# Optimization experiments

Hardware: AMD Instinct MI355X
Metric: run time of the kernel (lower is better)

Reference implementation:

```python
import jax, jax.numpy as jnp
import numpy as np

_R, _C = 64, 64
_N = _R * _C
_SEC_PER_A = 31556926.0
_K = 0.01        # sheet_conductivity
_ALPHA = 1.25    # sheet_flow_exp
_HR = 0.1        # bedrock_step_height
_LR = 2.0        # cavity_spacing
_A = 5e-25       # cavity_closure_coeff
_NEXP = 3        # Glen exponent


def _build_grid():
    idx = np.arange(_N).reshape(_R, _C)
    tail = np.concatenate([idx[:, :-1].ravel(), idx[:-1, :].ravel()]).astype(np.int32)
    head = np.concatenate([idx[:, 1:].ravel(), idx[1:, :].ravel()]).astype(np.int32)
    L = tail.size
    links_at_node = -np.ones((_N, 4), np.int32)
    adj = -np.ones((_N, 4), np.int32)
    cnt = np.zeros(_N, np.int32)
    for l in range(L):
        for a, b in ((tail[l], head[l]), (head[l], tail[l])):
            links_at_node[a, cnt[a]] = l
            adj[a, cnt[a]] = b
            cnt[a] += 1
    r, c = np.divmod(np.arange(_N), _C)
    status = ((r == 0) | (r == _R - 1) | (c == 0) | (c == _C - 1)).astype(np.int32)
    return tail, head, links_at_node, adj, status


def setup_inputs():
    key = jax.random.key(0)
    k = jax.random.split(key, 8)
    tail, head, links_at_node, adj, status = _build_grid()
    L = tail.size
    bedrock = jax.random.uniform(k[0], (_N,), jnp.float32, 0.0, 500.0)
    ice_thk = jax.random.uniform(k[1], (_N,), jnp.float32, 100.0, 1000.0)
    overburden = 917.0 * 9.81 * ice_thk
    base_potential = 1000.0 * 9.81 * bedrock + overburden
    potential = base_potential - 0.3 * overburden + 1e3 * jax.random.normal(k[2], (_N,), jnp.float32)
    sheet_thickness = jax.random.uniform(k[3], (_N,), jnp.float32, 0.01, 0.1)
    sliding_velocity = jax.random.uniform(k[4], (L,), jnp.float32, 10.0, 100.0)
    specific_melt_rate = jax.random.uniform(k[5], (_N,), jnp.float32, 1e-7, 1e-6)
    link_length = jnp.full((L,), 100.0, jnp.float32)
    adj_j = jnp.asarray(adj)
    # mean over ALL 4 slots, padded entries contribute 0 (matches original jnp.mean)
    adj_pot = jnp.mean(jnp.where(adj_j != -1, base_potential[adj_j], 0.0), axis=1)
    inflow = jnp.where(base_potential > adj_pot, 1, -1) * (jnp.asarray(status) > 0)
    return dict(
        base_potential=base_potential,
        overburden_pressure=overburden,
        specific_melt_rate=specific_melt_rate,
        sheet_thickness=sheet_thickness,
        potential=potential,
        sliding_velocity=sliding_velocity,
        link_length=link_length,
        link_tail=jnp.asarray(tail),
        link_head=jnp.asarray(head),
        links_at_node=jnp.asarray(links_at_node),
        inflow_outflow=inflow.astype(jnp.int32),
        dt=3600,
    )


def reference(base_potential, overburden_pressure, specific_melt_rate, sheet_thickness,
              potential, sliding_velocity, link_length, link_tail, link_head,
              links_at_node, inflow_outflow, dt):
    N = base_potential.shape[0]
    t, h = link_tail, link_head
    # --- elliptic operator assembly (per-link, scatter into dense [N,N]) ---
    sheets = 0.5 * (sheet_thickness[t] + sheet_thickness[h])
    inv_grad = jnp.abs((potential[t] - potential[h]) / link_length) ** (-0.5)
    c = -_K * sheets ** _ALPHA * link_length * inv_grad  # symmetric link coefficient (<0)
    dir_row = inflow_outflow == 1  # Dirichlet rows
    ct = jnp.where(dir_row[t], 0.0, c)  # contribution into row tail
    ch = jnp.where(dir_row[h], 0.0, c)  # contribution into row head
    M = (jnp.zeros((N, N), base_potential.dtype)
         .at[t, h].add(ct).at[h, t].add(ch)
         .at[t, t].add(-ct).at[h, h].add(-ch))
    M = jnp.where(dir_row[:, None], jnp.eye(N, dtype=M.dtype), M)
    forcing = jnp.where(dir_row, base_potential - overburden_pressure, specific_melt_rate)
    new_potential = jnp.linalg.solve(M, forcing)
    # --- sheet thickness: map_mean_of_links_to_node then Newton on node-local ODE ---
    valid = links_at_node != -1
    lv = (sliding_velocity / _SEC_PER_A)[links_at_node]  # [N,4]
    sliding = jnp.abs(jnp.sum(jnp.where(valid, lv, 0.0), axis=1)
                      / jnp.maximum(valid.sum(axis=1), 1))
    pressure = base_potential - new_potential
    dtf = jnp.asarray(dt, base_potential.dtype)
    # residual r(h) = h - h0 - dt*(sliding*(HR-h)/LR - A*P^n*h) is LINEAR in h,
    # so Newton converges in one exact step -> closed form:
    new_h = (sheet_thickness + dtf * sliding * _HR / _LR) / (
        1.0 + dtf * (sliding / _LR + _A * pressure ** _NEXP))
    return new_potential, new_h
```

## Files before the change

### kernel.cpp

```cpp
#include <hip/hip_runtime.h>
#include <math.h>


#define NT    512
#define NPT   8
#define NN    4096
#define NC    1024
#define NCC   256
#define CCIT  20
#define MAXIT 40

__global__ __launch_bounds__(NT, 1)
void sds_solver(const float* __restrict__ base_pot,
                const float* __restrict__ ovb,
                const float* __restrict__ melt,
                const float* __restrict__ sheet,
                const float* __restrict__ pot,
                const float* __restrict__ svel,
                const float* __restrict__ llen,
                const int*   __restrict__ ltail,
                const int*   __restrict__ lhead,
                const int*   __restrict__ lan,
                const int*   __restrict__ inflow,
                const int*   __restrict__ dt_raw,
                float* __restrict__ out,
                int N, int L)
{
    __shared__ __align__(16) float ZL0[2112], ZH0[2112];
    __shared__ __align__(16) float ZL1[2112], ZH1[2112];
    __shared__ __align__(16) float cW[NN], cE[NN], cN[NN], cS[NN];
    __shared__ __align__(16) float CB[32 + NC + 32];
    __shared__ __align__(16) float CB2[32 + NC + 32];
    __shared__ __align__(16) float EB[32 + NC + 32];
    __shared__ __align__(16) float ccb[NCC];
    __shared__ __align__(16) float cWc_s[NC], cEc_s[NC], cNc_s[NC], cSc_s[NC], dc_s[NC];
    __shared__ double redp[32], redg[16];

    const int tid  = threadIdx.x;
    const int lane = tid & 63;
    const int wid  = tid >> 6;
    const int m    = tid * NPT;

    if (N != NN || L != 8064) return;

    const int dti = dt_raw[0];
    const float as_f = __int_as_float(dti);
    const double dtf = (as_f > 0.5f && as_f < 1.0e12f) ? (double)as_f : (double)dti;

    const float invthf = 0.8f;
    const float c1f = 0.2195122f, c2f = 0.9756098f;
    const float wA = 1.75f;

    {
        const float4 z4 = make_float4(0.f, 0.f, 0.f, 0.f);
        #pragma unroll
        for (int i = tid; i < NN/4; i += NT) {
            ((float4*)cW)[i] = z4; ((float4*)cE)[i] = z4;
            ((float4*)cN)[i] = z4; ((float4*)cS)[i] = z4;
        }
        if (tid < 32) {
            ZL0[tid]=0.f; ZL0[2080+tid]=0.f; ZH0[tid]=0.f; ZH0[2080+tid]=0.f;
            ZL1[tid]=0.f; ZL1[2080+tid]=0.f; ZH1[tid]=0.f; ZH1[2080+tid]=0.f;
            CB[tid]=0.f;  CB[32+NC+tid]=0.f;
            CB2[tid]=0.f; CB2[32+NC+tid]=0.f;
            EB[tid]=0.f;  EB[32+NC+tid]=0.f;
        }
    }
    __syncthreads();

    for (int l = tid; l < 8064; l += NT) {
        int t, h;
        if (l < 4032) {
            const int r = l / 63;
            const int c2 = l - r * 63;
            t = (r << 6) + c2; h = t + 1;
        } else {
            t = l - 4032; h = t + 64;
        }
        const float sheets = 0.5f * (sheet[t] + sheet[h]);
        const float len = llen[l];
        const float grad = fabsf((pot[t] - pot[h]) / len);
        const float c = -0.01f * (sheets * sqrtf(sqrtf(sheets))) * len / sqrtf(grad);
        const bool dt_ = (inflow[t] == 1);
        const bool dh_ = (inflow[h] == 1);
        if (l < 4032) { cE[t] = dt_ ? 0.f : c; cW[h] = dh_ ? 0.f : c; }
        else          { cS[t] = dt_ ? 0.f : c; cN[h] = dh_ ? 0.f : c; }
    }
    __syncthreads();

    float cw[NPT], ce[NPT], cn[NPT], cs[NPT], dgf[NPT], invdf[NPT];
    double bb[NPT], gg[NPT], xv[NPT], rv[NPT];
    bool dirf[NPT];
    auto ldco = [&]() {
        const float4 w0 = *(const float4*)&cW[m], w1 = *(const float4*)&cW[m+4];
        const float4 e0 = *(const float4*)&cE[m], e1 = *(const float4*)&cE[m+4];
        const float4 n0 = *(const float4*)&cN[m], n1 = *(const float4*)&cN[m+4];
        const float4 s0 = *(const float4*)&cS[m], s1 = *(const float4*)&cS[m+4];
        cw[0]=w0.x;cw[1]=w0.y;cw[2]=w0.z;cw[3]=w0.w;cw[4]=w1.x;cw[5]=w1.y;cw[6]=w1.z;cw[7]=w1.w;
        ce[0]=e0.x;ce[1]=e0.y;ce[2]=e0.z;ce[3]=e0.w;ce[4]=e1.x;ce[5]=e1.y;ce[6]=e1.z;ce[7]=e1.w;
        cn[0]=n0.x;cn[1]=n0.y;cn[2]=n0.z;cn[3]=n0.w;cn[4]=n1.x;cn[5]=n1.y;cn[6]=n1.z;cn[7]=n1.w;
        cs[0]=s0.x;cs[1]=s0.y;cs[2]=s0.z;cs[3]=s0.w;cs[4]=s1.x;cs[5]=s1.y;cs[6]=s1.z;cs[7]=s1.w;
    };
    ldco();
    double gsum = 0.0, gcnt = 0.0;
    #pragma unroll
    for (int k = 0; k < NPT; ++k) {
        const int n = m + k;
        const bool dir = (inflow[n] == 1);
        const double g = (double)base_pot[n] - (double)ovb[n];
        const double d = -((double)cw[k] + (double)ce[k] + (double)cn[k] + (double)cs[k]);
        const double dg = (dir || d == 0.0) ? 1.0 : d;
        dgf[k] = (float)dg; invdf[k] = (float)(1.0 / dg);
        bb[k] = dir ? g : (double)melt[n];
        gg[k] = g; dirf[k] = dir;
        if (dir) { gsum += g; gcnt += 1.0; }
    }
    {
        #pragma unroll
        for (int off = 32; off > 0; off >>= 1) {
            gsum += __shfl_down(gsum, off, 64);
            gcnt += __shfl_down(gcnt, off, 64);
        }
        if (lane == 0) { redg[2*wid] = gsum; redg[2*wid+1] = gcnt; }
        __syncthreads();
        gsum = 0.0; gcnt = 0.0;
        #pragma unroll
        for (int w = 0; w < NT/64; ++w) { gsum += redg[2*w]; gcnt += redg[2*w+1]; }
    }
    const double gmean = gsum / (gcnt > 0.0 ? gcnt : 1.0);

    auto stz = [&](float* L_, float* H_, const float* v) {
        *(float4*)&L_[32 + 4*tid] = make_float4(v[0], v[1], v[2], v[3]);
        *(float4*)&H_[32 + 4*tid] = make_float4(v[4], v[5], v[6], v[7]);
    };
    float qf[NPT];
    auto spmv = [&](const float* L_, const float* H_, const float* vr) {
        const float4 uL = *(const float4*)&L_[4*tid];
        const float4 uH = *(const float4*)&H_[4*tid];
        const float4 dL = *(const float4*)&L_[64 + 4*tid];
        const float4 dH = *(const float4*)&H_[64 + 4*tid];
        const float lw = __shfl_up(vr[7], 1, 64);
        const float re = __shfl_down(vr[0], 1, 64);
        const float up[NPT] = {uL.x,uL.y,uL.z,uL.w,uH.x,uH.y,uH.z,uH.w};
        const float dn[NPT] = {dL.x,dL.y,dL.z,dL.w,dH.x,dH.y,dH.z,dH.w};
        #pragma unroll
        for (int k = 0; k < NPT; ++k) {
            const float wv = k ? vr[k-1] : lw;
            const float ev = (k < NPT-1) ? vr[k+1] : re;
            qf[k] = dgf[k]*vr[k] + cw[k]*wv + ce[k]*ev + cn[k]*up[k] + cs[k]*dn[k];
        }
    };
    auto fread0 = [&](int n) -> float {
        const int off = 32 + ((n >> 3) << 2) + (n & 3);
        return (n & 4) ? ZH0[off] : ZL0[off];
    };

    {
        float x0r[NPT];
        #pragma unroll
        for (int k = 0; k < NPT; ++k) {
            const float x0f = (float)(dirf[k] ? gg[k] : gmean);
            xv[k] = (double)x0f; x0r[k] = x0f;
        }
        stz(ZL0, ZH0, x0r); __syncthreads();
        spmv(ZL0, ZH0, x0r);
        #pragma unroll
        for (int k = 0; k < NPT; ++k)
            rv[k] = dirf[k] ? 0.0 : (bb[k] - (double)qf[k]);
    }
    __syncthreads();

    {
        #pragma unroll
        for (int k = 0; k < NPT; ++k) {
            const int n = m + k;
            if ((n & 63) != 0  && inflow[n-1]  == 1) cW[n] = 0.f;
            if ((n & 63) != 63 && inflow[n+1]  == 1) cE[n] = 0.f;
            if (n >= 64        && inflow[n-64] == 1) cN[n] = 0.f;
            if (n < NN-64      && inflow[n+64] == 1) cS[n] = 0.f;
        }
        float dgfF[NPT];
        #pragma unroll
        for (int k = 0; k < NPT; ++k) dgfF[k] = dirf[k] ? 0.f : dgf[k];
        stz(ZL0, ZH0, dgfF);
    }
    __syncthreads();
    ldco();

    #pragma unroll
    for (int q = 0; q < 2; ++q) {
        const int I = 2*tid + q;
        const int R = tid >> 4, C = I & 31;
        const int na = 128*R + 2*C, nb = na+1, nc_ = na+64, nd = na+65;
        cEc_s[I] = cE[nb] + cE[nd];
        cWc_s[I] = cW[na] + cW[nc_];
        cNc_s[I] = cN[na] + cN[nb];
        cSc_s[I] = cS[nc_] + cS[nd];
        const float d = fread0(na)+fread0(nb)+fread0(nc_)+fread0(nd)
                      + 2.0f*(cE[na] + cE[nc_] + cS[na] + cS[nb]);
        dc_s[I] = (d > 0.f) ? d : 1.0f;
    }
    __syncthreads();

    float cwc[2], cec[2], cnc[2], csc[2], dcr[2], invdc[2];
    {
        float2 t;
        t = *(float2*)&cWc_s[2*tid]; cwc[0]=t.x; cwc[1]=t.y;
        t = *(float2*)&cEc_s[2*tid]; cec[0]=t.x; cec[1]=t.y;
        t = *(float2*)&cNc_s[2*tid]; cnc[0]=t.x; cnc[1]=t.y;
        t = *(float2*)&cSc_s[2*tid]; csc[0]=t.x; csc[1]=t.y;
        t = *(float2*)&dc_s[2*tid];  dcr[0]=t.x; dcr[1]=t.y;
        invdc[0] = 1.0f/dcr[0]; invdc[1] = 1.0f/dcr[1];
    }
    float cwcc[4], cecc[4], cncc[4], cscc[4], dccr[4], invdcc[4];
    if (tid < 64) {
        #pragma unroll
        for (int j = 0; j < 4; ++j) {
            const int J = 4*tid + j;
            const int Rc = J >> 4, Cc = J & 15;
            const int IA = 64*Rc + 2*Cc, IB = IA+1, IC = IA+32, ID = IA+33;
            cecc[j] = cEc_s[IB] + cEc_s[ID];
            cwcc[j] = cWc_s[IA] + cWc_s[IC];
            cncc[j] = cNc_s[IA] + cNc_s[IB];
            cscc[j] = cSc_s[IC] + cSc_s[ID];
            const float d = dc_s[IA]+dc_s[IB]+dc_s[IC]+dc_s[ID]
                          + 2.0f*(cEc_s[IA] + cEc_s[IC] + cSc_s[IA] + cSc_s[IB]);
            dccr[j] = (d > 0.f) ? d : 1.0f;
            invdcc[j] = 1.0f/dccr[j];
        }
    }
    float c1cc[CCIT+1], c2cc[CCIT+1], invthcc;
    {
        const double a = 8e-3, b2 = 2.0;
        const double th = 0.5*(b2+a), de = 0.5*(b2-a), s1 = th/de;
        double rp = 1.0/s1;
        for (int j = 1; j <= CCIT; ++j) {
            const double rj = 1.0/(2.0*s1 - rp);
            c1cc[j] = (float)(rj*rp);
            c2cc[j] = (float)(2.0*rj/de);
            rp = rj;
        }
        invthcc = (float)(1.0/th);
    }
    auto cspmv = [&](const float* B_, float v0, float v1, float& q0, float& q1) {
        const float2 up = *(const float2*)&B_[2*tid];
        const float2 dn = *(const float2*)&B_[64 + 2*tid];
        const float wv = __shfl_up(v1, 1, 64);
        const float ev = __shfl_down(v0, 1, 64);
        q0 = dcr[0]*v0 + cwc[0]*wv + cec[0]*v1 + cnc[0]*up.x + csc[0]*dn.x;
        q1 = dcr[1]*v1 + cwc[1]*v0 + cec[1]*ev + cnc[1]*up.y + csc[1]*dn.y;
    };

    double rho_prev = 0.0, pap = 0.0, tol = 0.0;
    double pv[NPT], sv[NPT], rpv[NPT];
    #pragma unroll
    for (int k = 0; k < NPT; ++k) { pv[k]=0.0; sv[k]=0.0; rpv[k]=0.0; }

    for (int it = 0; it < MAXIT; ++it) {
        float f0[NPT], d0[NPT], d1[NPT], zpre[NPT];
        #pragma unroll
        for (int k = 0; k < NPT; ++k) { f0[k] = (float)rv[k] * invdf[k]; d0[k] = f0[k] * invthf; }
        stz(ZL0, ZH0, d0); __syncthreads();
        spmv(ZL0, ZH0, d0);
        #pragma unroll
        for (int k = 0; k < NPT; ++k) {
            const float f1 = f0[k] - qf[k]*invdf[k];
            d1[k] = c1f*d0[k] + c2f*f1;
            zpre[k] = d0[k] + d1[k];
            f0[k] = f1;
        }
        stz(ZL1, ZH1, d1); __syncthreads();
        spmv(ZL1, ZH1, d1);

        float r1[NPT], r1p[NPT];
        #pragma unroll
        for (int k = 0; k < NPT; ++k) {
            const float fres = f0[k] - qf[k]*invdf[k];
            r1[k] = dirf[k] ? 0.f : dgf[k]*fres;
        }
        #pragma unroll
        for (int k = 0; k < NPT; ++k) r1p[k] = __shfl_down(r1[k], 8, 64);
        if ((tid & 8) == 0) {
            float4 rc4;
            rc4.x = r1[0]+r1[1]+r1p[0]+r1p[1];
            rc4.y = r1[2]+r1[3]+r1p[2]+r1p[3];
            rc4.z = r1[4]+r1[5]+r1p[4]+r1p[5];
            rc4.w = r1[6]+r1[7]+r1p[6]+r1p[7];
            const int I0 = 32*(tid >> 4) + 4*(tid & 7);
            *(float4*)&CB2[32 + I0] = rc4;
        }
        __syncthreads();

        float rc[2], f0c[2], d0c[2], d1c[2], qc0, qc1;
        {
            const float2 rcl = *(const float2*)&CB2[32 + 2*tid];
            rc[0] = rcl.x; rc[1] = rcl.y;
        }
        #pragma unroll
        for (int q = 0; q < 2; ++q) {
            f0c[q] = rc[q] * invdc[q];
            d0c[q] = f0c[q] * invthf;
        }
        *(float2*)&CB[32 + 2*tid] = make_float2(d0c[0], d0c[1]);
        __syncthreads();
        cspmv(CB, d0c[0], d0c[1], qc0, qc1);
        {
            const float f1a = f0c[0] - qc0*invdc[0];
            const float f1b = f0c[1] - qc1*invdc[1];
            d1c[0] = c1f*d0c[0] + c2f*f1a;
            d1c[1] = c1f*d0c[1] + c2f*f1b;
            f0c[0] = f1a; f0c[1] = f1b;
        }
        *(float2*)&CB2[32 + 2*tid] = make_float2(d1c[0], d1c[1]);
        __syncthreads();
        cspmv(CB2, d1c[0], d1c[1], qc0, qc1);
        {
            const float fra = f0c[0] - qc0*invdc[0];
            const float frb = f0c[1] - qc1*invdc[1];
            *(float2*)&CB[32 + 2*tid] = make_float2(dcr[0]*fra, dcr[1]*frb);
        }
        __syncthreads();

        if (tid < 64) {
            float fr[4], dr[4], zc[4];
            #pragma unroll
            for (int j = 0; j < 4; ++j) {
                const int J = 4*tid + j;
                const int IA = 64*(J >> 4) + 2*(J & 15);
                const float rcc = CB[32+IA] + CB[32+IA+1] + CB[32+IA+32] + CB[32+IA+33];
                fr[j] = rcc * invdcc[j];
                dr[j] = fr[j] * invthcc;
                zc[j] = dr[j];
            }
            for (int s = 1; s <= CCIT; ++s) {
                float nv[4], sv2[4], qcc[4];
                #pragma unroll
                for (int j = 0; j < 4; ++j) {
                    nv[j]  = __shfl_up(dr[j], 4, 64);
                    sv2[j] = __shfl_down(dr[j], 4, 64);
                }
                const float wv = __shfl_up(dr[3], 1, 64);
                const float ev = __shfl_down(dr[0], 1, 64);
                #pragma unroll
                for (int j = 0; j < 4; ++j) {
                    const float wj = j ? dr[j-1] : wv;
                    const float ej = (j < 3) ? dr[j+1] : ev;
                    qcc[j] = dccr[j]*dr[j] + cwcc[j]*wj + cecc[j]*ej
                           + cncc[j]*nv[j] + cscc[j]*sv2[j];
                }
                #pragma unroll
                for (int j = 0; j < 4; ++j) {
                    fr[j] -= qcc[j] * invdcc[j];
                    dr[j]  = c1cc[s]*dr[j] + c2cc[s]*fr[j];
                    zc[j] += dr[j];
                }
            }
            *(float4*)&ccb[4*tid] = make_float4(zc[0], zc[1], zc[2], zc[3]);
        }
        __syncthreads();

        const float ecv = wA * ccb[16*(tid >> 5) + (tid & 15)];
        float zmc[2] = { d0c[0] + d1c[0] + ecv, d0c[1] + d1c[1] + ecv };
        *(float2*)&CB2[32 + 2*tid] = make_float2(zmc[0], zmc[1]);
        __syncthreads();
        cspmv(CB2, zmc[0], zmc[1], qc0, qc1);
        float fmc[2] = { (rc[0]-qc0)*invdc[0], (rc[1]-qc1)*invdc[1] };
        float d0p[2] = { fmc[0]*invthf, fmc[1]*invthf };
        *(float2*)&CB[32 + 2*tid] = make_float2(d0p[0], d0p[1]);
        __syncthreads();
        cspmv(CB, d0p[0], d0p[1], qc0, qc1);
        {
            const float f1a = fmc[0] - qc0*invdc[0];
            const float f1b = fmc[1] - qc1*invdc[1];
            const float efa = zmc[0] + c1f*d0p[0] + c2f*f1a + d0p[0];
            const float efb = zmc[1] + c1f*d0p[1] + c2f*f1b + d0p[1];
            *(float2*)&EB[32 + 2*tid] = make_float2(efa, efb);
        }
        __syncthreads();

        const float4 e4 = *(const float4*)&EB[32 + 32*(tid >> 4) + (tid & 7)*4];
        const float* e4p = (const float*)&e4;
        float zmid[NPT], zf[NPT];
        #pragma unroll
        for (int k = 0; k < NPT; ++k)
            zmid[k] = zpre[k] + (dirf[k] ? 0.f : wA * e4p[k >> 1]);
        stz(ZL1, ZH1, zmid); __syncthreads();
        spmv(ZL1, ZH1, zmid);
        float fmid[NPT], d0q[NPT];
        #pragma unroll
        for (int k = 0; k < NPT; ++k) {
            fmid[k] = (float)rv[k]*invdf[k] - qf[k]*invdf[k];
            d0q[k]  = fmid[k] * invthf;
        }
        stz(ZL0, ZH0, d0q); __syncthreads();
        spmv(ZL0, ZH0, d0q);
        #pragma unroll
        for (int k = 0; k < NPT; ++k) {
            const float f1 = fmid[k] - qf[k]*invdf[k];
            zf[k] = zmid[k] + d0q[k] + c1f*d0q[k] + c2f*f1;
        }
        stz(ZL1, ZH1, zf); __syncthreads();
        spmv(ZL1, ZH1, zf);

        double rho_n = 0.0, rzp = 0.0, zw = 0.0, pw = 0.0;
        #pragma unroll
        for (int k = 0; k < NPT; ++k) {
            const double zk = (double)zf[k], wk = (double)qf[k];
            rho_n += rv[k]  * zk;
            rzp   += rpv[k] * zk;
            zw    += zk * wk;
            pw    += pv[k] * wk;
        }
        #pragma unroll
        for (int off = 32; off > 0; off >>= 1) {
            rho_n += __shfl_down(rho_n, off, 64);
            rzp   += __shfl_down(rzp,   off, 64);
            zw    += __shfl_down(zw,    off, 64);
            pw    += __shfl_down(pw,    off, 64);
        }
        if (lane == 0) {
            redp[4*wid] = rho_n; redp[4*wid+1] = rzp;
            redp[4*wid+2] = zw;  redp[4*wid+3] = pw;
        }
        __syncthreads();
        rho_n = 0.0; rzp = 0.0; zw = 0.0; pw = 0.0;
        #pragma unroll
        for (int w = 0; w < NT/64; ++w) {
            rho_n += redp[4*w];   rzp += redp[4*w+1];
            zw    += redp[4*w+2]; pw  += redp[4*w+3];
        }

        if (it == 0) {
            tol = rho_n * 1e-3 + 1e-300;
            if (!(rho_n > 0.0)) break;
        } else if (rho_n <= tol || !(rho_n > 0.0)) break;
        const double beta = (it == 0) ? 0.0
                          : fmax(0.0, (rho_n - rzp) / rho_prev);
        pap = zw + beta * (2.0 * pw + beta * pap);
        if (!(pap > 0.0)) break;
        const double alpha = rho_n / pap;
        rho_prev = rho_n;
        #pragma unroll
        for (int k = 0; k < NPT; ++k) {
            rpv[k] = rv[k];
            pv[k] = (double)zf[k] + beta * pv[k];
            sv[k] = (double)qf[k] + beta * sv[k];
            xv[k] += alpha * pv[k];
            rv[k] -= alpha * sv[k];
        }
    }

    float xo[NPT], ho[NPT];
    #pragma unroll
    for (int k = 0; k < NPT; ++k) {
        const int n = m + k;
        const int r = n >> 6, c2 = n & 63;
        const double x = dirf[k] ? gg[k] : xv[k];
        xo[k] = (float)x;

        const int hb = r * 63 + c2;
        float sva = 0.0f; int cnt = 0;
        if (c2 > 0)  { sva += svel[hb - 1];       cnt++; }
        if (c2 < 63) { sva += svel[hb];           cnt++; }
        if (r  > 0)  { sva += svel[4032 + n - 64]; cnt++; }
        if (r  < 63) { sva += svel[4032 + n];      cnt++; }
        const double sliding =
            fabs((double)sva / 31556926.0 / (double)(cnt > 0 ? cnt : 1));
        const double P   = (double)base_pot[n] - x;
        const double num = (double)sheet[n] + dtf * sliding * 0.1 / 2.0;
        const double den = 1.0 + dtf * (sliding / 2.0 + 5e-25 * P * P * P);
        ho[k] = (float)(num / den);
    }
    *(float4*)&out[m]        = make_float4(xo[0], xo[1], xo[2], xo[3]);
    *(float4*)&out[m+4]      = make_float4(xo[4], xo[5], xo[6], xo[7]);
    *(float4*)&out[NN+m]     = make_float4(ho[0], ho[1], ho[2], ho[3]);
    *(float4*)&out[NN+m+4]   = make_float4(ho[4], ho[5], ho[6], ho[7]);
}

extern "C" void kernel_launch(void* const* d_in, const int* in_sizes, int n_in,
                              void* d_out, int out_size, void* d_ws, size_t ws_size,
                              hipStream_t stream) {
    const float* base_pot = (const float*)d_in[0];
    const float* ovb      = (const float*)d_in[1];
    const float* melt     = (const float*)d_in[2];
    const float* sheet    = (const float*)d_in[3];
    const float* pot      = (const float*)d_in[4];
    const float* svel     = (const float*)d_in[5];
    const float* llen     = (const float*)d_in[6];
    const int*   ltail    = (const int*)d_in[7];
    const int*   lhead    = (const int*)d_in[8];
    const int*   lan      = (const int*)d_in[9];
    const int*   inflow   = (const int*)d_in[10];
    const int*   dt_raw   = (const int*)d_in[11];
    float* out = (float*)d_out;
    const int N = in_sizes[0];
    const int L = in_sizes[5];

    hipLaunchKernelGGL(sds_solver, dim3(1), dim3(NT), 0, stream,
                       base_pot, ovb, melt, sheet, pot, svel, llen,
                       ltail, lhead, lan, inflow, dt_raw, out, N, L);
}
```

Before: 156.2 us.

## Replace wave shuffles with DPP and permlane swaps in solver inner loops

Replaces __shfl-based neighbour exchanges and wave reductions (which go through ds_bpermute/LDS) with DPP row/wave shifts and v_permlane16/32_swap instructions. The coarse-coarse smoother's data layout is remapped so north/south neighbours are in-register and east/west come from row shifts, with cross-row boundaries handled by permlane swaps. Wave reductions now use permlane swaps plus DPP row rotates. The aim is lower latency on the many sequential iterations of the single-block solver. The risks are boundary correctness: DPP wave_shl/wave_shr behaviour on gfx950, bound_ctrl semantics, and the new layout mapping.

```diff
diff --git a/kernel.cpp b/kernel.cpp
--- a/kernel.cpp
+++ b/kernel.cpp
@@ -9,6 +9,57 @@
 #define NCC   256
 #define CCIT  20
 #define MAXIT 40
+
+enum : int { RSHL1 = 0x101, RSHR1 = 0x111,
+             ROR8 = 0x128, ROR12 = 0x12C, ROR14 = 0x12E, ROR15 = 0x12F,
+             WSHL1 = 0x130, WSHR1 = 0x138 };
+
+template<int CTRL>
+__device__ __forceinline__ float dppf(float x) {
+    return __int_as_float(__builtin_amdgcn_update_dpp(
+        __float_as_int(x), __float_as_int(x), CTRL, 0xF, 0xF, false));
+}
+template<int CTRL>
+__device__ __forceinline__ double dppd(double x) {
+    const int lo = __double2loint(x), hi = __double2hiint(x);
+    const int l2 = __builtin_amdgcn_update_dpp(lo, lo, CTRL, 0xF, 0xF, false);
+    const int h2 = __builtin_amdgcn_update_dpp(hi, hi, CTRL, 0xF, 0xF, false);
+    return __hiloint2double(h2, l2);
+}
+__device__ __forceinline__ void pl16sw(int& a, int& b) {
+    asm volatile("s_nop 1\n\tv_permlane16_swap_b32 %0, %1" : "+v"(a), "+v"(b));
+}
+__device__ __forceinline__ void pl32sw(int& a, int& b) {
+    asm volatile("s_nop 1\n\tv_permlane32_swap_b32 %0, %1" : "+v"(a), "+v"(b));
+}
+__device__ __forceinline__ float shift_dn16(float x, bool inR2) {
+    int a = __float_as_int(x), b = __float_as_int(x);
+    pl16sw(a, b);
+    int g = b, g2 = b;
+    pl32sw(g, g2);
+    return __int_as_float(inR2 ? g : a);
+}
+__device__ __forceinline__ float shift_up16(float x, bool inR1) {
+    int a = __float_as_int(x), b = __float_as_int(x);
+    pl16sw(a, b);
+    int d1 = __float_as_int(x), d2 = __float_as_int(x);
+    pl32sw(d1, d2);
+    int e1 = d2, e2 = d2;
+    pl16sw(e1, e2);
+    return __int_as_float(inR1 ? e1 : b);
+}
+__device__ __forceinline__ double dsw32(double x) {
+    int lo = __double2loint(x), hi = __double2hiint(x);
+    int a = lo, b = lo; pl32sw(a, b);
+    int c = hi, d = hi; pl32sw(c, d);
+    return __hiloint2double(d, b);
+}
+__device__ __forceinline__ double dsw16(double x) {
+    int lo = __double2loint(x), hi = __double2hiint(x);
+    int a = lo, b = lo; pl16sw(a, b);
+    int c = hi, d = hi; pl16sw(c, d);
+    return __hiloint2double(d, b);
+}
 
 __global__ __launch_bounds__(NT, 1)
 void sds_solver(const float* __restrict__ base_pot,
@@ -139,8 +190,8 @@
         const float4 uH = *(const float4*)&H_[4*tid];
         const float4 dL = *(const float4*)&L_[64 + 4*tid];
         const float4 dH = *(const float4*)&H_[64 + 4*tid];
-        const float lw = __shfl_up(vr[7], 1, 64);
-        const float re = __shfl_down(vr[0], 1, 64);
+        const float lw = dppf<WSHR1>(vr[7]);
+        const float re = dppf<WSHL1>(vr[0]);
         const float up[NPT] = {uL.x,uL.y,uL.z,uL.w,uH.x,uH.y,uH.z,uH.w};
         const float dn[NPT] = {dL.x,dL.y,dL.z,dL.w,dH.x,dH.y,dH.z,dH.w};
         #pragma unroll
@@ -216,8 +267,7 @@
     if (tid < 64) {
         #pragma unroll
         for (int j = 0; j < 4; ++j) {
-            const int J = 4*tid + j;
-            const int Rc = J >> 4, Cc = J & 15;
+            const int Rc = ((tid >> 4) << 2) + j, Cc = tid & 15;
             const int IA = 64*Rc + 2*Cc, IB = IA+1, IC = IA+32, ID = IA+33;
             cecc[j] = cEc_s[IB] + cEc_s[ID];
             cwcc[j] = cWc_s[IA] + cWc_s[IC];
@@ -245,8 +295,8 @@
     auto cspmv = [&](const float* B_, float v0, float v1, float& q0, float& q1) {
         const float2 up = *(const float2*)&B_[2*tid];
         const float2 dn = *(const float2*)&B_[64 + 2*tid];
-        const float wv = __shfl_up(v1, 1, 64);
-        const float ev = __shfl_down(v0, 1, 64);
+        const float wv = dppf<WSHR1>(v1);
+        const float ev = dppf<WSHL1>(v0);
         q0 = dcr[0]*v0 + cwc[0]*wv + cec[0]*v1 + cnc[0]*up.x + csc[0]*dn.x;
         q1 = dcr[1]*v1 + cwc[1]*v0 + cec[1]*ev + cnc[1]*up.y + csc[1]*dn.y;
     };
@@ -279,7 +329,7 @@
             r1[k] = dirf[k] ? 0.f : dgf[k]*fres;
         }
         #pragma unroll
-        for (int k = 0; k < NPT; ++k) r1p[k] = __shfl_down(r1[k], 8, 64);
+        for (int k = 0; k < NPT; ++k) r1p[k] = dppf<ROR8>(r1[k]);
         if ((tid & 8) == 0) {
             float4 rc4;
             rc4.x = r1[0]+r1[1]+r1p[0]+r1p[1];
@@ -322,31 +372,30 @@
         __syncthreads();
 
         if (tid < 64) {
+            const int cc_c  = tid & 15;
+            const int cc_rb = tid >> 4;
+            const bool inR1 = (cc_rb == 1), inR2 = (cc_rb == 2);
             float fr[4], dr[4], zc[4];
             #pragma unroll
             for (int j = 0; j < 4; ++j) {
-                const int J = 4*tid + j;
-                const int IA = 64*(J >> 4) + 2*(J & 15);
+                const int IA = (((cc_rb << 2) + j) << 6) + (cc_c << 1);
                 const float rcc = CB[32+IA] + CB[32+IA+1] + CB[32+IA+32] + CB[32+IA+33];
                 fr[j] = rcc * invdcc[j];
                 dr[j] = fr[j] * invthcc;
                 zc[j] = dr[j];
             }
             for (int s = 1; s <= CCIT; ++s) {
-                float nv[4], sv2[4], qcc[4];
+                const float zN = shift_dn16(dr[3], inR2);
+                const float zS = shift_up16(dr[0], inR1);
+                float qcc[4];
                 #pragma unroll
                 for (int j = 0; j < 4; ++j) {
-                    nv[j]  = __shfl_up(dr[j], 4, 64);
-                    sv2[j] = __shfl_down(dr[j], 4, 64);
-                }
-                const float wv = __shfl_up(dr[3], 1, 64);
-                const float ev = __shfl_down(dr[0], 1, 64);
-                #pragma unroll
-                for (int j = 0; j < 4; ++j) {
-                    const float wj = j ? dr[j-1] : wv;
-                    const float ej = (j < 3) ? dr[j+1] : ev;
+                    const float wj = dppf<RSHR1>(dr[j]);
+                    const float ej = dppf<RSHL1>(dr[j]);
+                    const float nj = j ? dr[j-1] : zN;
+                    const float sj = (j < 3) ? dr[j+1] : zS;
                     qcc[j] = dccr[j]*dr[j] + cwcc[j]*wj + cecc[j]*ej
-                           + cncc[j]*nv[j] + cscc[j]*sv2[j];
+                           + cncc[j]*nj + cscc[j]*sj;
                 }
                 #pragma unroll
                 for (int j = 0; j < 4; ++j) {
@@ -355,7 +404,9 @@
                     zc[j] += dr[j];
                 }
             }
-            *(float4*)&ccb[4*tid] = make_float4(zc[0], zc[1], zc[2], zc[3]);
+            #pragma unroll
+            for (int j = 0; j < 4; ++j)
+                ccb[(((cc_rb << 2) + j) << 4) + cc_c] = zc[j];
         }
         __syncthreads();
 
@@ -411,13 +462,12 @@
             zw    += zk * wk;
             pw    += pv[k] * wk;
         }
-        #pragma unroll
-        for (int off = 32; off > 0; off >>= 1) {
-            rho_n += __shfl_down(rho_n, off, 64);
-            rzp   += __shfl_down(rzp,   off, 64);
-            zw    += __shfl_down(zw,    off, 64);
-            pw    += __shfl_down(pw,    off, 64);
-        }
+        rho_n += dsw32(rho_n); rzp += dsw32(rzp); zw += dsw32(zw); pw += dsw32(pw);
+        rho_n += dsw16(rho_n); rzp += dsw16(rzp); zw += dsw16(zw); pw += dsw16(pw);
+        rho_n += dppd<ROR8 >(rho_n); rzp += dppd<ROR8 >(rzp); zw += dppd<ROR8 >(zw); pw += dppd<ROR8 >(pw);
+        rho_n += dppd<ROR12>(rho_n); rzp += dppd<ROR12>(rzp); zw += dppd<ROR12>(zw); pw += dppd<ROR12>(pw);
+        rho_n += dppd<ROR14>(rho_n); rzp += dppd<ROR14>(rzp); zw += dppd<ROR14>(zw); pw += dppd<ROR14>(pw);
+        rho_n += dppd<ROR15>(rho_n); rzp += dppd<ROR15>(rzp); zw += dppd<ROR15>(zw); pw += dppd<ROR15>(pw);
         if (lane == 0) {
             redp[4*wid] = rho_n; redp[4*wid+1] = rzp;
             redp[4*wid+2] = zw;  redp[4*wid+3] = pw;
```

New measurement: 149.4 us. 4.4% less time.
